# Optimization experiments

Measured on AMD Instinct MI355X. Metric: run time of the kernel, lower is better.

## Reference

```python
import jax, jax.numpy as jnp
import numpy as np

N_ENTITY = 100000
N_RELATION = 64
DIM = 16
N_HOP = 2
N_MEM = 32
N_NODES = 16384


def setup_inputs() -> dict:
    key = jax.random.key(0)
    ks = jax.random.split(key, 7)
    return {
        "nodes": jax.random.randint(ks[0], (N_NODES,), 0, N_ENTITY),
        "memories_h": jax.random.randint(ks[1], (N_HOP, N_NODES, N_MEM), 0, N_ENTITY),
        "memories_r": jax.random.randint(ks[2], (N_HOP, N_NODES, N_MEM), 0, N_RELATION),
        "memories_t": jax.random.randint(ks[3], (N_HOP, N_NODES, N_MEM), 0, N_ENTITY),
        "entity_emb": jax.random.normal(ks[4], (N_ENTITY, DIM), jnp.float32) * 0.1,
        "relation_emb": jax.random.normal(ks[5], (N_RELATION, DIM * DIM), jnp.float32) * 0.1,
        "W": jax.random.normal(ks[6], (DIM, DIM), jnp.float32) * 0.1,
    }


def reference(nodes, memories_h, memories_r, memories_t, entity_emb, relation_emb, W):
    # item embeddings for the query nodes: [N, D]
    item = entity_emb[nodes]
    o_list = []
    for hop in range(N_HOP):  # small fixed hop count (2)
        h = entity_emb[memories_h[hop]]                                  # [N, M, D]
        r = relation_emb[memories_r[hop]].reshape(-1, N_MEM, DIM, DIM)   # [N, M, D, D]
        t = entity_emb[memories_t[hop]]                                  # [N, M, D]
        # Rh = R @ h : [N, M, D]
        Rh = jnp.einsum('nmde,nme->nmd', r, h)
        # attention over the n_memory slots (softmax dim=0 per node in original)
        probs = jax.nn.softmax(jnp.einsum('nmd,nd->nm', Rh, item), axis=1)
        # weighted sum of tails: [N, D]
        o = jnp.einsum('nm,nmd->nd', probs, t)
        # item_update_mode == 'plus_transform': Linear(dim, dim, bias=False)
        item = (item + o) @ W.T
        o_list.append(o)
    # Faithful to the original torch in-place semantics: at hop 0 the line
    # `kg_feature += o_list[0]` doubles o0 in place; the final result for
    # n_hop=2 is therefore o1 + 2*o0.
    return o_list[1] + 2.0 * o_list[0]
```

## Files before the change

kernel.cpp:

```cpp
#include <hip/hip_runtime.h>

#define NE     100000
#define NR     64
#define DIM    16
#define NHOP   2
#define NMEM   32
#define NNODES 16384

#define WPITCH 20

typedef __attribute__((ext_vector_type(2))) _Float16 half2_t;

static __device__ __forceinline__ half2_t as_h2(unsigned u) {
    union { unsigned i; half2_t h; } c; c.i = u; return c.h;
}

static __device__ __forceinline__ float qdot2(unsigned u, unsigned ip, float q) {
#if __has_builtin(__builtin_amdgcn_fdot2)
    return __builtin_amdgcn_fdot2(as_h2(u), as_h2(ip), q, false);
#else
    half2_t a = as_h2(u), b = as_h2(ip);
    return q + (float)a.x * (float)b.x + (float)a.y * (float)b.y;
#endif
}

static __device__ __forceinline__ float dpp_sum16(float v) {
    union { int i; float f; } a, b;
    a.f = v;
    b.i = __builtin_amdgcn_update_dpp(0, a.i, 0xB1,  0xf, 0xf, true); a.f += b.f;
    b.i = __builtin_amdgcn_update_dpp(0, a.i, 0x4E,  0xf, 0xf, true); a.f += b.f;
    b.i = __builtin_amdgcn_update_dpp(0, a.i, 0x124, 0xf, 0xf, true); a.f += b.f;
    b.i = __builtin_amdgcn_update_dpp(0, a.i, 0x128, 0xf, 0xf, true); a.f += b.f;
    return a.f;
}

static __device__ __forceinline__ float bcast(float v, int l) {
    return __int_as_float(__builtin_amdgcn_readlane(__float_as_int(v), l));
}

static __device__ __forceinline__ unsigned short f2h(float f) {
    union { _Float16 h; unsigned short s; } c; c.h = (_Float16)f; return c.s;
}

static __device__ __forceinline__ unsigned pack2h(float a, float b) {
    union { _Float16 h[2]; unsigned u; } c;
    c.h[0] = (_Float16)a; c.h[1] = (_Float16)b;
    return c.u;
}

extern "C" __global__ void __launch_bounds__(512, 8)
ripple_kernel(const int* __restrict__ nodes,
              const int* __restrict__ mh,
              const int* __restrict__ mr,
              const int* __restrict__ mt,
              const float* __restrict__ ent,
              const float* __restrict__ rel,
              const float* __restrict__ W,
              float* __restrict__ out)
{
    __shared__ __align__(16) unsigned short rt[NR * 256];
    __shared__ __align__(16) float ws[DIM * WPITCH];

    const int tid = threadIdx.x;

    {
        const float4* rel4 = (const float4*)rel;
        #pragma unroll
        for (int i = 0; i < 8; ++i) {
            int vidx = i * 512 + tid;
            float4 v = rel4[vidx];
            int k0 = vidx * 4;
            int r  = k0 >> 8;
            int k  = k0 & 255;
            int d  = k >> 4;
            int e0 = k & 15;
            int phys = ((d >> 2) + (e0 >> 2)) & 3;
            unsigned short* p = &rt[r * 256 + e0 * 16 + phys * 4 + (d & 3)];
            p[0]  = f2h(v.x);
            p[16] = f2h(v.y);
            p[32] = f2h(v.z);
            p[48] = f2h(v.w);
        }
        if (tid < 256) ws[(tid >> 4) * WPITCH + (tid & 15)] = W[tid];
    }
    __syncthreads();

    const int lane = tid & 63;
    const int wid  = tid >> 6;
    const int g    = lane >> 4;
    const int e    = lane & 15;
    const int n    = blockIdx.x * 8 + wid;

    int voff[4];
    {
        const int s = e >> 2;
        #pragma unroll
        for (int j = 0; j < 4; ++j)
            voff[j] = e * 32 + (((j + s) & 3) << 3);
    }

    float item    = ent[nodes[n] * DIM + e];
    float out_acc = 0.f;

    #pragma unroll
    for (int hop = 0; hop < NHOP; ++hop) {
        unsigned ip[8];
        #pragma unroll
        for (int j = 0; j < 8; ++j)
            ip[j] = pack2h(bcast(item, 2 * j), bcast(item, 2 * j + 1));

        const int ibase = hop * (NNODES * NMEM) + n * NMEM + g * 8;
        int hi[8], ri[8], ti[8];
        {
            const int4* p;
            p = (const int4*)(mh + ibase); ((int4*)hi)[0] = p[0]; ((int4*)hi)[1] = p[1];
            p = (const int4*)(mr + ibase); ((int4*)ri)[0] = p[0]; ((int4*)ri)[1] = p[1];
            p = (const int4*)(mt + ibase); ((int4*)ti)[0] = p[0]; ((int4*)ti)[1] = p[1];
        }

        float hv[8], tv[8];
        #pragma unroll
        for (int it = 0; it < 8; ++it) {
            hv[it] = ent[hi[it] * DIM + e];
            tv[it] = ent[ti[it] * DIM + e];
        }

        float sc[8];
        #pragma unroll
        for (int it = 0; it < 8; ++it) {
            const char* rbase = (const char*)rt + (ri[it] << 9);
            float q = 0.f;
            #pragma unroll
            for (int j = 0; j < 4; ++j) {
                uint2 u = *(const uint2*)(rbase + voff[j]);
                q = qdot2(u.x, ip[2 * j + 0], q);
                q = qdot2(u.y, ip[2 * j + 1], q);
            }
            sc[it] = dpp_sum16(q * hv[it]);
        }

        float Z = 0.f;
        #pragma unroll
        for (int it = 0; it < 8; ++it) { sc[it] = __expf(sc[it]); Z += sc[it]; }
        Z += __shfl_xor(Z, 16);
        Z += __shfl_xor(Z, 32);
        const float inv = 1.f / Z;

        float o = 0.f;
        #pragma unroll
        for (int it = 0; it < 8; ++it) o += sc[it] * tv[it];
        o *= inv;
        o += __shfl_xor(o, 16);
        o += __shfl_xor(o, 32);

        out_acc += (hop == 0) ? 2.f * o : o;

        const float v = item + o;
        float nit = 0.f;
        const float4* wr = (const float4*)&ws[e * WPITCH];
        #pragma unroll
        for (int j = 0; j < 4; ++j) {
            float4 w = wr[j];
            nit += w.x * bcast(v, 4 * j + 0) + w.y * bcast(v, 4 * j + 1)
                 + w.z * bcast(v, 4 * j + 2) + w.w * bcast(v, 4 * j + 3);
        }
        item = nit;
    }

    if (lane < 16) out[n * DIM + e] = out_acc;
}

extern "C" void kernel_launch(void* const* d_in, const int* in_sizes, int n_in,
                              void* d_out, int out_size, void* d_ws, size_t ws_size,
                              hipStream_t stream) {
    const int*   nodes = (const int*)d_in[0];
    const int*   mh    = (const int*)d_in[1];
    const int*   mr    = (const int*)d_in[2];
    const int*   mt    = (const int*)d_in[3];
    const float* ent   = (const float*)d_in[4];
    const float* rel   = (const float*)d_in[5];
    const float* W     = (const float*)d_in[6];
    float*       out   = (float*)d_out;

    dim3 grid(NNODES / 8);
    dim3 block(512);
    ripple_kernel<<<grid, block, 0, stream>>>(nodes, mh, mr, mt, ent, rel, W, out);
}
```

Measured before the change: 103.5 us.

## Quantize relation matrices and item to int8 and use sdot4 dot products

Relation matrices are quantized to int8 in shared memory with one scale per block (the global max over all relations), and the item vector is quantized to int8 per hop. The R·item products then run as packed sdot4 integer dot products instead of fp16 fdot2. The shared-memory layout gets a padded per-column pitch, and the gather and softmax loops are fused into one streaming loop. This halves LDS traffic and dot-product instruction count, but adds a block-wide max reduction and an extra barrier at setup, and lowers numerical accuracy.

```diff
diff --git a/kernel.cpp b/kernel.cpp
--- a/kernel.cpp
+++ b/kernel.cpp
@@ -7,20 +7,21 @@
 #define NMEM   32
 #define NNODES 16384
 
+#define COLP   24
+#define RELP   392
 #define WPITCH 20
 
-typedef __attribute__((ext_vector_type(2))) _Float16 half2_t;
-
-static __device__ __forceinline__ half2_t as_h2(unsigned u) {
-    union { unsigned i; half2_t h; } c; c.i = u; return c.h;
-}
-
-static __device__ __forceinline__ float qdot2(unsigned u, unsigned ip, float q) {
-#if __has_builtin(__builtin_amdgcn_fdot2)
-    return __builtin_amdgcn_fdot2(as_h2(u), as_h2(ip), q, false);
+static __device__ __forceinline__ int sdot4(unsigned a, unsigned b, int c) {
+#if __has_builtin(__builtin_amdgcn_sdot4)
+    return __builtin_amdgcn_sdot4((int)a, (int)b, c, false);
 #else
-    half2_t a = as_h2(u), b = as_h2(ip);
-    return q + (float)a.x * (float)b.x + (float)a.y * (float)b.y;
+    #pragma unroll
+    for (int k = 0; k < 4; ++k) {
+        int xa = (int)((a >> (8 * k)) & 0xffu); xa = (xa ^ 0x80) - 0x80;
+        int xb = (int)((b >> (8 * k)) & 0xffu); xb = (xb ^ 0x80) - 0x80;
+        c += xa * xb;
+    }
+    return c;
 #endif
 }
 
@@ -33,19 +34,18 @@
     b.i = __builtin_amdgcn_update_dpp(0, a.i, 0x128, 0xf, 0xf, true); a.f += b.f;
     return a.f;
 }
+static __device__ __forceinline__ float dpp_max16(float v) {
+    union { int i; float f; } a, b;
+    a.f = v;
+    b.i = __builtin_amdgcn_update_dpp(0, a.i, 0xB1,  0xf, 0xf, true); a.f = fmaxf(a.f, b.f);
+    b.i = __builtin_amdgcn_update_dpp(0, a.i, 0x4E,  0xf, 0xf, true); a.f = fmaxf(a.f, b.f);
+    b.i = __builtin_amdgcn_update_dpp(0, a.i, 0x124, 0xf, 0xf, true); a.f = fmaxf(a.f, b.f);
+    b.i = __builtin_amdgcn_update_dpp(0, a.i, 0x128, 0xf, 0xf, true); a.f = fmaxf(a.f, b.f);
+    return a.f;
+}
 
 static __device__ __forceinline__ float bcast(float v, int l) {
     return __int_as_float(__builtin_amdgcn_readlane(__float_as_int(v), l));
-}
-
-static __device__ __forceinline__ unsigned short f2h(float f) {
-    union { _Float16 h; unsigned short s; } c; c.h = (_Float16)f; return c.s;
-}
-
-static __device__ __forceinline__ unsigned pack2h(float a, float b) {
-    union { _Float16 h[2]; unsigned u; } c;
-    c.h[0] = (_Float16)a; c.h[1] = (_Float16)b;
-    return c.u;
 }
 
 extern "C" __global__ void __launch_bounds__(512, 8)
@@ -58,30 +58,55 @@
               const float* __restrict__ W,
               float* __restrict__ out)
 {
-    __shared__ __align__(16) unsigned short rt[NR * 256];
-    __shared__ __align__(16) float ws[DIM * WPITCH];
+    __shared__ __align__(16) char  rt[NR * RELP];
+    __shared__ __align__(16) float ws[DIM * WPITCH + 8];
 
     const int tid = threadIdx.x;
 
+    float vbuf[32];
     {
-        const float4* rel4 = (const float4*)rel;
+        float m = 0.f;
         #pragma unroll
         for (int i = 0; i < 8; ++i) {
-            int vidx = i * 512 + tid;
-            float4 v = rel4[vidx];
-            int k0 = vidx * 4;
-            int r  = k0 >> 8;
-            int k  = k0 & 255;
-            int d  = k >> 4;
-            int e0 = k & 15;
-            int phys = ((d >> 2) + (e0 >> 2)) & 3;
-            unsigned short* p = &rt[r * 256 + e0 * 16 + phys * 4 + (d & 3)];
-            p[0]  = f2h(v.x);
-            p[16] = f2h(v.y);
-            p[32] = f2h(v.z);
-            p[48] = f2h(v.w);
-        }
+            int T = i * 512 + tid;
+            int r = T >> 6, e = (T >> 2) & 15, d0 = (T & 3) << 2;
+            const float* p = rel + r * 256 + d0 * 16 + e;
+            float a = p[0], b = p[16], c = p[32], d = p[48];
+            vbuf[4 * i + 0] = a; vbuf[4 * i + 1] = b;
+            vbuf[4 * i + 2] = c; vbuf[4 * i + 3] = d;
+            m = fmaxf(m, fmaxf(fmaxf(fabsf(a), fabsf(b)), fmaxf(fabsf(c), fabsf(d))));
+        }
+        #pragma unroll
+        for (int off = 32; off; off >>= 1) m = fmaxf(m, __shfl_xor(m, off));
+        if ((tid & 63) == 0) ws[DIM * WPITCH + (tid >> 6)] = m;
         if (tid < 256) ws[(tid >> 4) * WPITCH + (tid & 15)] = W[tid];
+    }
+    __syncthreads();
+
+    float smax;
+    {
+        float m = 1e-30f;
+        #pragma unroll
+        for (int j = 0; j < 8; ++j) m = fmaxf(m, ws[DIM * WPITCH + j]);
+        smax = m;
+    }
+    const float rs = smax * (1.f / 127.f);
+
+    {
+        const float qs = 127.f / smax;
+        #pragma unroll
+        for (int i = 0; i < 8; ++i) {
+            int T = i * 512 + tid;
+            int r = T >> 6, e = (T >> 2) & 15, d0 = (T & 3) << 2;
+            unsigned pk = 0;
+            #pragma unroll
+            for (int j = 0; j < 4; ++j) {
+                int q = (int)rintf(vbuf[4 * i + j] * qs);
+                q = q < -127 ? -127 : (q > 127 ? 127 : q);
+                pk |= ((unsigned)q & 0xffu) << (8 * j);
+            }
+            *(unsigned*)&rt[r * RELP + e * COLP + d0] = pk;
+        }
     }
     __syncthreads();
 
@@ -91,67 +116,56 @@
     const int e    = lane & 15;
     const int n    = blockIdx.x * 8 + wid;
 
-    int voff[4];
-    {
-        const int s = e >> 2;
-        #pragma unroll
-        for (int j = 0; j < 4; ++j)
-            voff[j] = e * 32 + (((j + s) & 3) << 3);
-    }
-
     float item    = ent[nodes[n] * DIM + e];
     float out_acc = 0.f;
 
     #pragma unroll
     for (int hop = 0; hop < NHOP; ++hop) {
-        unsigned ip[8];
-        #pragma unroll
-        for (int j = 0; j < 8; ++j)
-            ip[j] = pack2h(bcast(item, 2 * j), bcast(item, 2 * j + 1));
+        const float mx  = fmaxf(dpp_max16(fabsf(item)), 1e-30f);
+        int q8 = (int)rintf(item * (127.f / mx));
+        q8 = q8 < -127 ? -127 : (q8 > 127 ? 127 : q8);
+        unsigned ip[4];
+        #pragma unroll
+        for (int j = 0; j < 4; ++j) {
+            unsigned b0 = (unsigned)__builtin_amdgcn_readlane(q8, 4 * j + 0) & 0xffu;
+            unsigned b1 = (unsigned)__builtin_amdgcn_readlane(q8, 4 * j + 1) & 0xffu;
+            unsigned b2 = (unsigned)__builtin_amdgcn_readlane(q8, 4 * j + 2) & 0xffu;
+            unsigned b3 = (unsigned)__builtin_amdgcn_readlane(q8, 4 * j + 3) & 0xffu;
+            ip[j] = b0 | (b1 << 8) | (b2 << 16) | (b3 << 24);
+        }
+        const float cq = rs * mx * (1.f / 127.f);
 
         const int ibase = hop * (NNODES * NMEM) + n * NMEM + g * 8;
         int hi[8], ri[8], ti[8];
         {
             const int4* p;
-            p = (const int4*)(mh + ibase); ((int4*)hi)[0] = p[0]; ((int4*)hi)[1] = p[1];
-            p = (const int4*)(mr + ibase); ((int4*)ri)[0] = p[0]; ((int4*)ri)[1] = p[1];
-            p = (const int4*)(mt + ibase); ((int4*)ti)[0] = p[0]; ((int4*)ti)[1] = p[1];
-        }
-
-        float hv[8], tv[8];
+            p = (const int4*)(mh + ibase); *(int4*)&hi[0] = p[0]; *(int4*)&hi[4] = p[1];
+            p = (const int4*)(mr + ibase); *(int4*)&ri[0] = p[0]; *(int4*)&ri[4] = p[1];
+            p = (const int4*)(mt + ibase); *(int4*)&ti[0] = p[0]; *(int4*)&ti[4] = p[1];
+        }
+
+        float Z = 0.f, o = 0.f;
         #pragma unroll
         for (int it = 0; it < 8; ++it) {
-            hv[it] = ent[hi[it] * DIM + e];
-            tv[it] = ent[ti[it] * DIM + e];
-        }
-
-        float sc[8];
-        #pragma unroll
-        for (int it = 0; it < 8; ++it) {
-            const char* rbase = (const char*)rt + (ri[it] << 9);
-            float q = 0.f;
-            #pragma unroll
-            for (int j = 0; j < 4; ++j) {
-                uint2 u = *(const uint2*)(rbase + voff[j]);
-                q = qdot2(u.x, ip[2 * j + 0], q);
-                q = qdot2(u.y, ip[2 * j + 1], q);
-            }
-            sc[it] = dpp_sum16(q * hv[it]);
-        }
-
-        float Z = 0.f;
-        #pragma unroll
-        for (int it = 0; it < 8; ++it) { sc[it] = __expf(sc[it]); Z += sc[it]; }
+            const char* cb = rt + ri[it] * RELP + e * COLP;
+            uint2 u0 = *(const uint2*)cb;
+            uint2 u1 = *(const uint2*)(cb + 8);
+            int acc = sdot4(u1.y, ip[3],
+                      sdot4(u1.x, ip[2],
+                      sdot4(u0.y, ip[1],
+                      sdot4(u0.x, ip[0], 0))));
+            float hv = ent[hi[it] * DIM + e];
+            float sc = dpp_sum16((float)acc * cq * hv);
+            float ex = __expf(sc);
+            float tv = ent[ti[it] * DIM + e];
+            Z += ex;
+            o += ex * tv;
+        }
         Z += __shfl_xor(Z, 16);
         Z += __shfl_xor(Z, 32);
-        const float inv = 1.f / Z;
-
-        float o = 0.f;
-        #pragma unroll
-        for (int it = 0; it < 8; ++it) o += sc[it] * tv[it];
-        o *= inv;
         o += __shfl_xor(o, 16);
         o += __shfl_xor(o, 32);
+        o *= 1.f / Z;
 
         out_acc += (hop == 0) ? 2.f * o : o;
 
```

Result: no change. 104.2 us (+0.7%).

## Pre-quantize entity table to fp16 and fuse softmax accumulation loop

Applied to the files above, without the earlier changes.

Adds a pre-pass kernel that converts the full entity embedding table to fp16 in the workspace, so the main kernel's random gathers read 32-byte rows instead of 64-byte rows. The softmax is restructured to accumulate the exp sum and the weighted tail sum inside the score loop, and the normalization moves after the cross-group reduction. The pre-pass reads and writes the whole 6.4 MB table on every call, which is more data than the gathers themselves touch. fp16 storage also lowers precision of item, head and tail values.

```diff
diff --git a/kernel.cpp b/kernel.cpp
--- a/kernel.cpp
+++ b/kernel.cpp
@@ -41,11 +41,22 @@
 static __device__ __forceinline__ unsigned short f2h(float f) {
     union { _Float16 h; unsigned short s; } c; c.h = (_Float16)f; return c.s;
 }
-
 static __device__ __forceinline__ unsigned pack2h(float a, float b) {
     union { _Float16 h[2]; unsigned u; } c;
     c.h[0] = (_Float16)a; c.h[1] = (_Float16)b;
     return c.u;
+}
+
+extern "C" __global__ void __launch_bounds__(256)
+ent_quant_kernel(const float* __restrict__ ent, _Float16* __restrict__ et, int n4) {
+    int i = blockIdx.x * 256 + threadIdx.x;
+    if (i < n4) {
+        float4 v = ((const float4*)ent)[i];
+        union { _Float16 h[4]; unsigned long long u; } c;
+        c.h[0] = (_Float16)v.x; c.h[1] = (_Float16)v.y;
+        c.h[2] = (_Float16)v.z; c.h[3] = (_Float16)v.w;
+        *(unsigned long long*)(et + 4 * (long long)i) = c.u;
+    }
 }
 
 extern "C" __global__ void __launch_bounds__(512, 8)
@@ -53,7 +64,7 @@
               const int* __restrict__ mh,
               const int* __restrict__ mr,
               const int* __restrict__ mt,
-              const float* __restrict__ ent,
+              const _Float16* __restrict__ et,
               const float* __restrict__ rel,
               const float* __restrict__ W,
               float* __restrict__ out)
@@ -99,7 +110,7 @@
             voff[j] = e * 32 + (((j + s) & 3) << 3);
     }
 
-    float item    = ent[nodes[n] * DIM + e];
+    float item    = (float)et[nodes[n] * DIM + e];
     float out_acc = 0.f;
 
     #pragma unroll
@@ -113,21 +124,19 @@
         int hi[8], ri[8], ti[8];
         {
             const int4* p;
-            p = (const int4*)(mh + ibase); ((int4*)hi)[0] = p[0]; ((int4*)hi)[1] = p[1];
-            p = (const int4*)(mr + ibase); ((int4*)ri)[0] = p[0]; ((int4*)ri)[1] = p[1];
-            p = (const int4*)(mt + ibase); ((int4*)ti)[0] = p[0]; ((int4*)ti)[1] = p[1];
+            p = (const int4*)(mh + ibase); *(int4*)&hi[0] = p[0]; *(int4*)&hi[4] = p[1];
+            p = (const int4*)(mr + ibase); *(int4*)&ri[0] = p[0]; *(int4*)&ri[4] = p[1];
+            p = (const int4*)(mt + ibase); *(int4*)&ti[0] = p[0]; *(int4*)&ti[4] = p[1];
         }
 
-        float hv[8], tv[8];
+        float hv[8];
+        #pragma unroll
+        for (int it = 0; it < 8; ++it) hv[it] = (float)et[hi[it] * DIM + e];
+
+        float Z = 0.f, o = 0.f;
         #pragma unroll
         for (int it = 0; it < 8; ++it) {
-            hv[it] = ent[hi[it] * DIM + e];
-            tv[it] = ent[ti[it] * DIM + e];
-        }
-
-        float sc[8];
-        #pragma unroll
-        for (int it = 0; it < 8; ++it) {
+            float tv = (float)et[ti[it] * DIM + e];
             const char* rbase = (const char*)rt + (ri[it] << 9);
             float q = 0.f;
             #pragma unroll
@@ -136,22 +145,16 @@
                 q = qdot2(u.x, ip[2 * j + 0], q);
                 q = qdot2(u.y, ip[2 * j + 1], q);
             }
-            sc[it] = dpp_sum16(q * hv[it]);
+            float sc = dpp_sum16(q * hv[it]);
+            float ex = __expf(sc);
+            Z += ex;
+            o += ex * tv;
         }
-
-        float Z = 0.f;
-        #pragma unroll
-        for (int it = 0; it < 8; ++it) { sc[it] = __expf(sc[it]); Z += sc[it]; }
         Z += __shfl_xor(Z, 16);
         Z += __shfl_xor(Z, 32);
-        const float inv = 1.f / Z;
-
-        float o = 0.f;
-        #pragma unroll
-        for (int it = 0; it < 8; ++it) o += sc[it] * tv[it];
-        o *= inv;
         o += __shfl_xor(o, 16);
         o += __shfl_xor(o, 32);
+        o *= 1.f / Z;
 
         out_acc += (hop == 0) ? 2.f * o : o;
 
@@ -181,8 +184,12 @@
     const float* rel   = (const float*)d_in[5];
     const float* W     = (const float*)d_in[6];
     float*       out   = (float*)d_out;
+    _Float16*    et    = (_Float16*)d_ws;
+
+    const int n4 = NE * DIM / 4;
+    ent_quant_kernel<<<(n4 + 255) / 256, 256, 0, stream>>>(ent, et, n4);
 
     dim3 grid(NNODES / 8);
     dim3 block(512);
-    ripple_kernel<<<grid, block, 0, stream>>>(nodes, mh, mr, mt, ent, rel, W, out);
+    ripple_kernel<<<grid, block, 0, stream>>>(nodes, mh, mr, mt, et, rel, W, out);
 }
```

New measurement: 100.2 us. 1.03x faster.
